# Performance work log

Measured on AMD Instinct MI355X. Metric: run time of the kernel, lower is better.

The kernel has to match this reference:

```python
import jax, jax.numpy as jnp
import numpy as np

NUM_EXPERTS = 8
TOP_K = 2
N_EMBD = 1024
BLOCKING = 128
D_FFN = ((4 * N_EMBD // TOP_K) + BLOCKING - 1) // BLOCKING * BLOCKING  # 2048


def setup_inputs() -> dict:
    key = jax.random.key(0)
    k_x, k_r, k_w1, k_w2 = jax.random.split(key, 4)
    B, S = 4, 2048
    x = jax.random.normal(k_x, (B, S, N_EMBD), dtype=jnp.float32)
    # nn.Linear weight layout: [out_features, in_features]
    router_w = jax.random.normal(k_r, (NUM_EXPERTS, N_EMBD), dtype=jnp.float32) * 0.02
    # trunc_normal(std=0.02, a=-0.06, b=0.06) approximated by clipped normal
    w1 = jnp.clip(jax.random.normal(k_w1, (N_EMBD, NUM_EXPERTS * D_FFN), dtype=jnp.float32) * 0.02, -0.06, 0.06)
    w2 = jnp.clip(jax.random.normal(k_w2, (NUM_EXPERTS * D_FFN, N_EMBD), dtype=jnp.float32) * 0.02, -0.06, 0.06)
    return {"x": x, "router_w": router_w, "w1": w1, "w2": w2}


def reference(x, router_w, w1, w2):
    B, S, D = x.shape
    T = B * S
    x_flat = x.reshape(T, D)

    # Router
    router_logits = x_flat @ router_w.T                       # [T, E]
    router_probs = jax.nn.softmax(router_logits.astype(jnp.float32), axis=-1)
    expert_weights, selected_experts = jax.lax.top_k(router_probs, TOP_K)  # [T, K]
    expert_weights = expert_weights / expert_weights.sum(axis=-1, keepdims=True)
    expert_weights = expert_weights.astype(x.dtype)

    # Combine weights c[t, e] = sum_k weight[t, k] * [sel[t, k] == e]
    combine = jnp.zeros((T, NUM_EXPERTS), dtype=x.dtype)
    combine = combine.at[jnp.arange(T)[:, None], selected_experts].add(expert_weights)

    # Expert FFNs (math equivalent of block-sparse sdd/gelu/dsd + scatter-combine)
    w1r = w1.reshape(D, NUM_EXPERTS, D_FFN)
    w2r = w2.reshape(NUM_EXPERTS, D_FFN, D)
    out_flat = jnp.zeros((T, D), dtype=x.dtype)
    for e in range(NUM_EXPERTS):
        h = jax.nn.gelu(x_flat @ w1r[:, e, :], approximate=False)  # [T, d_ffn]
        out_flat = out_flat + combine[:, e:e + 1] * (h @ w2r[e])
    output = out_flat.reshape(B, S, D)

    # Aux losses
    router_z_loss = jnp.mean(jax.nn.logsumexp(router_logits, axis=-1) ** 2)
    p_i = router_probs.mean(axis=0)                           # [E]
    f_i = jnp.zeros((NUM_EXPERTS,), dtype=x.dtype).at[selected_experts.reshape(-1)].add(
        jnp.float32(1.0) / (T * TOP_K))
    load_balance_loss = NUM_EXPERTS * jnp.dot(f_i, p_i.astype(x.dtype))

    return output, router_z_loss, load_balance_loss, f_i
```

## Files before the change

### kernel.cpp

```cpp
#include <hip/hip_runtime.h>
#include <hip/hip_bf16.h>
#include <math.h>

#define T_TOK   8192
#define D_MODEL 1024
#define DFFN    2048
#define N_EXP   8
#define NASSIGN (T_TOK*2)

#define BM 128
#define BN 128
#define BK 64
#define TILE_MAX 144

#define WS_ZSUM     0
#define WS_PSUM     4
#define WS_COUNTS   64
#define WS_CURSOR   96
#define WS_OFFS     128
#define WS_NTILES   160
#define WS_TMAP     256
#define WS_SEL      4096
#define WS_WGT      69632
#define WS_AIDX     135168
#define WS_AW       200704
#define WS_XB       266240
#define WS_W1T      (WS_XB + 16777216)
#define WS_W2T      (WS_W1T + 33554432)
#define WS_H        (WS_W2T + 33554432)

typedef __attribute__((ext_vector_type(8))) short bf16x8;
typedef __attribute__((ext_vector_type(4))) float f32x4;
typedef __attribute__((ext_vector_type(4))) unsigned int u32x4;

static __device__ __forceinline__ unsigned short f2bf(float f) {
    unsigned int u = __builtin_bit_cast(unsigned int, f);
    u += 0x7fffu + ((u >> 16) & 1u);
    return (unsigned short)(u >> 16);
}

static __device__ __forceinline__ void gll16(const unsigned short* g, unsigned short* l) {
    __builtin_amdgcn_global_load_lds(
        (const __attribute__((address_space(1))) unsigned int*)g,
        (__attribute__((address_space(3))) unsigned int*)l, 16, 0, 0);
}

static __device__ __forceinline__ int frag_off(int row, int kc) {
    return (row * 8 + (kc ^ (row & 7))) * 8;
}

__global__ __launch_bounds__(256) void transpose_cvt_kernel(
    const float* __restrict__ in, unsigned short* __restrict__ out, int K, int N)
{
    int e = blockIdx.z;
    const float* inp = in + (size_t)e * K * N;
    unsigned short* outp = out + (size_t)e * K * N;
    __shared__ unsigned short tile[64][68];
    int k0 = blockIdx.y * 64, n0 = blockIdx.x * 64;
    int tid = threadIdx.x;
    int r = tid >> 4, c4 = (tid & 15) * 4;
    #pragma unroll
    for (int p = 0; p < 4; ++p) {
        int k = r + p * 16;
        float4 v = *(const float4*)(inp + (size_t)(k0 + k) * N + n0 + c4);
        tile[k][c4+0] = f2bf(v.x);
        tile[k][c4+1] = f2bf(v.y);
        tile[k][c4+2] = f2bf(v.z);
        tile[k][c4+3] = f2bf(v.w);
    }
    __syncthreads();
    int n = tid >> 2, kc = (tid & 3) * 16;
    unsigned short t[16];
    #pragma unroll
    for (int j = 0; j < 16; ++j) t[j] = tile[kc + j][n];
    unsigned short* o = outp + (size_t)(n0 + n) * K + k0 + kc;
    *(u32x4*)o       = *(u32x4*)t;
    *(u32x4*)(o + 8) = *(u32x4*)(t + 8);
}

__global__ __launch_bounds__(256) void router_kernel(
    const float* __restrict__ x, const float* __restrict__ rw,
    float* zsum, float* psum, int* counts, int* sel, float* wgt,
    unsigned short* __restrict__ xb)
{
    __shared__ float xs[32*129];
    __shared__ float rs[8*129];
    __shared__ float lg[32*9];
    __shared__ float blk_p[8];
    __shared__ int   blk_c[8];
    __shared__ float blk_z;
    int tid = threadIdx.x;
    if (tid < 8) { blk_p[tid] = 0.f; blk_c[tid] = 0; }
    if (tid == 8) blk_z = 0.f;
    int tb = blockIdx.x * 32;
    int tt = tid >> 3, e = tid & 7;
    float acc = 0.f;
    for (int c = 0; c < 8; ++c) {
        int c0 = c * 128;
        #pragma unroll
        for (int p = 0; p < 16; ++p) {
            int flat = p * 256 + tid;
            int r = flat >> 7, col = flat & 127;
            xs[r*129 + col] = x[(size_t)(tb + r)*D_MODEL + c0 + col];
        }
        #pragma unroll
        for (int p = 0; p < 4; ++p) {
            int flat = p * 256 + tid;
            int er = flat >> 7, col = flat & 127;
            rs[er*129 + col] = rw[(size_t)er*D_MODEL + c0 + col];
        }
        __syncthreads();
        {
            int rr = tid >> 3, cc = (tid & 7) * 16;
            unsigned short tmp[16];
            #pragma unroll
            for (int j = 0; j < 16; ++j) tmp[j] = f2bf(xs[rr*129 + cc + j]);
            unsigned short* o = xb + (size_t)(tb + rr)*D_MODEL + c0 + cc;
            *(u32x4*)o       = *(u32x4*)tmp;
            *(u32x4*)(o + 8) = *(u32x4*)(tmp + 8);
        }
        #pragma unroll 8
        for (int i = 0; i < 128; ++i)
            acc += xs[tt*129 + i] * rs[e*129 + i];
        __syncthreads();
    }
    lg[tt*9 + e] = acc;
    __syncthreads();
    if (tid < 32) {
        int t = tb + tid;
        float l[8], p[8];
        float mx = -1e30f;
        #pragma unroll
        for (int j = 0; j < 8; ++j) { l[j] = lg[tid*9 + j]; mx = fmaxf(mx, l[j]); }
        float se = 0.f;
        #pragma unroll
        for (int j = 0; j < 8; ++j) { p[j] = expf(l[j] - mx); se += p[j]; }
        float inv = 1.f / se;
        #pragma unroll
        for (int j = 0; j < 8; ++j) p[j] *= inv;
        float lse = mx + logf(se);
        atomicAdd(&blk_z, lse*lse);
        #pragma unroll
        for (int j = 0; j < 8; ++j) atomicAdd(&blk_p[j], p[j]);
        int i0 = 0; float b0 = p[0];
        #pragma unroll
        for (int j = 1; j < 8; ++j) if (p[j] > b0) { b0 = p[j]; i0 = j; }
        int i1 = -1; float b1 = -1.f;
        #pragma unroll
        for (int j = 0; j < 8; ++j) if (j != i0 && p[j] > b1) { b1 = p[j]; i1 = j; }
        float s = b0 + b1;
        sel[t*2+0] = i0; sel[t*2+1] = i1;
        wgt[t*2+0] = b0 / s; wgt[t*2+1] = b1 / s;
        atomicAdd(&blk_c[i0], 1); atomicAdd(&blk_c[i1], 1);
    }
    __syncthreads();
    if (tid < 8) {
        atomicAdd(&counts[tid], blk_c[tid]);
        unsafeAtomicAdd(&psum[tid], blk_p[tid]);
    }
    if (tid == 8) unsafeAtomicAdd(zsum, blk_z);
}

__global__ void finalize_kernel(const int* counts, const float* psum, const float* zsum,
                                int* offs, int* ntiles, int* tmap, float* out_tail)
{
    if (threadIdx.x != 0) return;
    int off = 0, nt = 0;
    float lb = 0.f;
    for (int e = 0; e < N_EXP; ++e) {
        int c = counts[e];
        offs[e] = off;
        for (int m0 = 0; m0 < c; m0 += BM) {
            tmap[nt*4+0] = e;
            tmap[nt*4+1] = off + m0;
            tmap[nt*4+2] = min(BM, c - m0);
            tmap[nt*4+3] = 0;
            nt++;
        }
        float fi = (float)c / (float)NASSIGN;
        out_tail[2 + e] = fi;
        lb += fi * (psum[e] / (float)T_TOK);
        off += c;
    }
    *ntiles = nt;
    out_tail[0] = zsum[0] / (float)T_TOK;
    out_tail[1] = (float)N_EXP * lb;
}

__global__ __launch_bounds__(256) void scatter_kernel(
    const int* __restrict__ sel, const float* __restrict__ wgt,
    const int* __restrict__ offs, int* cursor, int* aidx, float* aw)
{
    int t = blockIdx.x * 256 + threadIdx.x;
    if (t >= T_TOK) return;
    #pragma unroll
    for (int k = 0; k < 2; ++k) {
        int e = sel[t*2 + k];
        int pos = atomicAdd(&cursor[e], 1);
        int r = offs[e] + pos;
        aidx[r] = t;
        aw[r] = wgt[t*2 + k];
    }
}

__global__ __launch_bounds__(256) void gemm1_kernel(
    const unsigned short* __restrict__ xb, const unsigned short* __restrict__ w1t,
    const int* __restrict__ aidx, const int* __restrict__ tmap,
    const int* __restrict__ ntiles, unsigned short* __restrict__ H)
{
    int tile = blockIdx.y;
    if (tile >= *ntiles) return;
    int e     = tmap[tile*4+0];
    int gr    = tmap[tile*4+1];
    int valid = tmap[tile*4+2];
    int n0 = blockIdx.x * BN;
    __shared__ unsigned short As[BM*BK];
    __shared__ unsigned short Bs[BN*BK];
    int tid = threadIdx.x;
    int lane = tid & 63, wave = tid >> 6;
    int wm = (wave & 1) * 64, wn = (wave >> 1) * 64;
    int q = lane >> 4, r16 = lane & 15;
    f32x4 acc[4][4];
    #pragma unroll
    for (int i = 0; i < 4; ++i)
        #pragma unroll
        for (int j = 0; j < 4; ++j) acc[i][j] = (f32x4){0.f, 0.f, 0.f, 0.f};

    const unsigned short* aga[4];
    const unsigned short* bga[4];
    unsigned short* ldsA[4];
    unsigned short* ldsB[4];
    #pragma unroll
    for (int j = 0; j < 4; ++j) {
        int c = tid + j*256;
        int m = c >> 3, kl = c & 7;
        int kg = kl ^ (m & 7);
        int tok = aidx[gr + min(m, valid - 1)];
        aga[j] = xb + (size_t)tok * D_MODEL + kg*8;
        bga[j] = w1t + ((size_t)(e * DFFN + n0 + m)) * D_MODEL + kg*8;
        ldsA[j] = As + c*8;
        ldsB[j] = Bs + c*8;
    }

    for (int kt = 0; kt < D_MODEL / BK; ++kt) {
        int ko = kt * BK;
        #pragma unroll
        for (int j = 0; j < 4; ++j) gll16(aga[j] + ko, ldsA[j]);
        #pragma unroll
        for (int j = 0; j < 4; ++j) gll16(bga[j] + ko, ldsB[j]);
        __syncthreads();
        #pragma unroll
        for (int kh = 0; kh < 2; ++kh) {
            bf16x8 af[4], bfr[4];
            #pragma unroll
            for (int im = 0; im < 4; ++im)
                af[im] = *(const bf16x8*)&As[frag_off(wm + im*16 + r16, q + 4*kh)];
            #pragma unroll
            for (int in = 0; in < 4; ++in)
                bfr[in] = *(const bf16x8*)&Bs[frag_off(wn + in*16 + r16, q + 4*kh)];
            #pragma unroll
            for (int im = 0; im < 4; ++im)
                #pragma unroll
                for (int in = 0; in < 4; ++in)
                    acc[im][in] = __builtin_amdgcn_mfma_f32_16x16x32_bf16(af[im], bfr[in], acc[im][in], 0, 0, 0);
        }
        __syncthreads();
    }
    #pragma unroll
    for (int im = 0; im < 4; ++im) {
        #pragma unroll
        for (int reg = 0; reg < 4; ++reg) {
            int m = wm + im*16 + q*4 + reg;
            if (m < valid) {
                size_t rowbase = (size_t)(gr + m) * DFFN + n0 + wn;
                #pragma unroll
                for (int in = 0; in < 4; ++in) {
                    float v = acc[im][in][reg];
                    float g = 0.5f * v * (1.0f + erff(v * 0.70710678118654752f));
                    H[rowbase + in*16 + r16] = f2bf(g);
                }
            }
        }
    }
}

__global__ __launch_bounds__(256) void gemm2_kernel(
    const unsigned short* __restrict__ H, const unsigned short* __restrict__ w2t,
    const int* __restrict__ aidx, const float* __restrict__ aw,
    const int* __restrict__ tmap, const int* __restrict__ ntiles,
    float* __restrict__ out)
{
    int tile = blockIdx.y;
    if (tile >= *ntiles) return;
    int e     = tmap[tile*4+0];
    int gr    = tmap[tile*4+1];
    int valid = tmap[tile*4+2];
    int n0 = blockIdx.x * BN;
    __shared__ unsigned short As[BM*BK];
    __shared__ unsigned short Bs[BN*BK];
    int tid = threadIdx.x;
    int lane = tid & 63, wave = tid >> 6;
    int wm = (wave & 1) * 64, wn = (wave >> 1) * 64;
    int q = lane >> 4, r16 = lane & 15;
    f32x4 acc[4][4];
    #pragma unroll
    for (int i = 0; i < 4; ++i)
        #pragma unroll
        for (int j = 0; j < 4; ++j) acc[i][j] = (f32x4){0.f, 0.f, 0.f, 0.f};

    const unsigned short* aga[4];
    const unsigned short* bga[4];
    unsigned short* ldsA[4];
    unsigned short* ldsB[4];
    #pragma unroll
    for (int j = 0; j < 4; ++j) {
        int c = tid + j*256;
        int m = c >> 3, kl = c & 7;
        int kg = kl ^ (m & 7);
        aga[j] = H + (size_t)(gr + min(m, valid - 1)) * DFFN + kg*8;
        bga[j] = w2t + (size_t)e * (DFFN * D_MODEL) + (size_t)(n0 + m) * DFFN + kg*8;
        ldsA[j] = As + c*8;
        ldsB[j] = Bs + c*8;
    }

    for (int kt = 0; kt < DFFN / BK; ++kt) {
        int ko = kt * BK;
        #pragma unroll
        for (int j = 0; j < 4; ++j) gll16(aga[j] + ko, ldsA[j]);
        #pragma unroll
        for (int j = 0; j < 4; ++j) gll16(bga[j] + ko, ldsB[j]);
        __syncthreads();
        #pragma unroll
        for (int kh = 0; kh < 2; ++kh) {
            bf16x8 af[4], bfr[4];
            #pragma unroll
            for (int im = 0; im < 4; ++im)
                af[im] = *(const bf16x8*)&As[frag_off(wm + im*16 + r16, q + 4*kh)];
            #pragma unroll
            for (int in = 0; in < 4; ++in)
                bfr[in] = *(const bf16x8*)&Bs[frag_off(wn + in*16 + r16, q + 4*kh)];
            #pragma unroll
            for (int im = 0; im < 4; ++im)
                #pragma unroll
                for (int in = 0; in < 4; ++in)
                    acc[im][in] = __builtin_amdgcn_mfma_f32_16x16x32_bf16(af[im], bfr[in], acc[im][in], 0, 0, 0);
        }
        __syncthreads();
    }
    #pragma unroll
    for (int im = 0; im < 4; ++im) {
        #pragma unroll
        for (int reg = 0; reg < 4; ++reg) {
            int m = wm + im*16 + q*4 + reg;
            if (m < valid) {
                int t = aidx[gr + m];
                float w = aw[gr + m];
                float* orow = out + (size_t)t*D_MODEL + n0 + wn;
                #pragma unroll
                for (int in = 0; in < 4; ++in)
                    unsafeAtomicAdd(&orow[in*16 + r16], w * acc[im][in][reg]);
            }
        }
    }
}

extern "C" void kernel_launch(void* const* d_in, const int* in_sizes, int n_in,
                              void* d_out, int out_size, void* d_ws, size_t ws_size,
                              hipStream_t stream)
{
    const float* x  = (const float*)d_in[0];
    const float* rw = (const float*)d_in[1];
    const float* w1 = (const float*)d_in[2];
    const float* w2 = (const float*)d_in[3];
    float* out = (float*)d_out;
    char* ws = (char*)d_ws;
    float* zsum   = (float*)(ws + WS_ZSUM);
    float* psum   = (float*)(ws + WS_PSUM);
    int*   counts = (int*)(ws + WS_COUNTS);
    int*   cursor = (int*)(ws + WS_CURSOR);
    int*   offs   = (int*)(ws + WS_OFFS);
    int*   ntiles = (int*)(ws + WS_NTILES);
    int*   tmap   = (int*)(ws + WS_TMAP);
    int*   sel    = (int*)(ws + WS_SEL);
    float* wgt    = (float*)(ws + WS_WGT);
    int*   aidx   = (int*)(ws + WS_AIDX);
    float* aw     = (float*)(ws + WS_AW);
    unsigned short* xb  = (unsigned short*)(ws + WS_XB);
    unsigned short* w1t = (unsigned short*)(ws + WS_W1T);
    unsigned short* w2t = (unsigned short*)(ws + WS_W2T);
    unsigned short* H   = (unsigned short*)(ws + WS_H);

    hipMemsetAsync(d_out, 0, (size_t)T_TOK * D_MODEL * sizeof(float), stream);
    hipMemsetAsync(ws, 0, 256, stream);

    transpose_cvt_kernel<<<dim3(16384/64, 1024/64, 1), 256, 0, stream>>>(w1, w1t, 1024, 16384);
    transpose_cvt_kernel<<<dim3(1024/64, 2048/64, 8), 256, 0, stream>>>(w2, w2t, 2048, 1024);

    router_kernel<<<T_TOK/32, 256, 0, stream>>>(x, rw, zsum, psum, counts, sel, wgt, xb);
    finalize_kernel<<<1, 64, 0, stream>>>(counts, psum, zsum, offs, ntiles, tmap,
                                          out + (size_t)T_TOK * D_MODEL);
    scatter_kernel<<<T_TOK/256, 256, 0, stream>>>(sel, wgt, offs, cursor, aidx, aw);
    gemm1_kernel<<<dim3(DFFN/BN, TILE_MAX), 256, 0, stream>>>(xb, w1t, aidx, tmap, ntiles, H);
    gemm2_kernel<<<dim3(D_MODEL/BN, TILE_MAX), 256, 0, stream>>>(H, w2t, aidx, aw, tmap, ntiles, out);
}
```

Measured before the change: 595.7 us.

## Double-buffer LDS in expert GEMMs and remap blocks for XCD locality

Both expert GEMM kernels now use double-buffered shared memory tiles: the next K-slice is prefetched with direct global-to-LDS loads while MFMAs run on the current slice, with explicit vmcnt waits and raw barriers in place of two __syncthreads per iteration. The grid is flattened to 1D and block IDs are remapped so that all N-tiles of a given row tile land on the same XCD, improving L2 reuse of the gathered activation rows. Wave priority is raised around the MFMA section. Doubling LDS per block lowers the number of resident blocks per CU, and the hand-written waitcnt counts assume eight outstanding loads per thread.

```diff
diff --git a/kernel.cpp b/kernel.cpp
--- a/kernel.cpp
+++ b/kernel.cpp
@@ -208,14 +208,17 @@
     const int* __restrict__ aidx, const int* __restrict__ tmap,
     const int* __restrict__ ntiles, unsigned short* __restrict__ H)
 {
-    int tile = blockIdx.y;
+    int bid = blockIdx.x;
+    int xcd = bid & 7;
+    int jj  = bid >> 3;
+    int tile = (jj >> 4) * 8 + xcd;
+    int n0   = (jj & 15) * BN;
     if (tile >= *ntiles) return;
     int e     = tmap[tile*4+0];
     int gr    = tmap[tile*4+1];
     int valid = tmap[tile*4+2];
-    int n0 = blockIdx.x * BN;
-    __shared__ unsigned short As[BM*BK];
-    __shared__ unsigned short Bs[BN*BK];
+    __shared__ unsigned short As[2][BM*BK];
+    __shared__ unsigned short Bs[2][BN*BK];
     int tid = threadIdx.x;
     int lane = tid & 63, wave = tid >> 6;
     int wm = (wave & 1) * 64, wn = (wave >> 1) * 64;
@@ -228,43 +231,62 @@
 
     const unsigned short* aga[4];
     const unsigned short* bga[4];
-    unsigned short* ldsA[4];
-    unsigned short* ldsB[4];
-    #pragma unroll
-    for (int j = 0; j < 4; ++j) {
-        int c = tid + j*256;
-        int m = c >> 3, kl = c & 7;
+    int coff[4];
+    #pragma unroll
+    for (int u = 0; u < 4; ++u) {
+        int cc = tid + u*256;
+        int m = cc >> 3, kl = cc & 7;
         int kg = kl ^ (m & 7);
         int tok = aidx[gr + min(m, valid - 1)];
-        aga[j] = xb + (size_t)tok * D_MODEL + kg*8;
-        bga[j] = w1t + ((size_t)(e * DFFN + n0 + m)) * D_MODEL + kg*8;
-        ldsA[j] = As + c*8;
-        ldsB[j] = Bs + c*8;
-    }
-
-    for (int kt = 0; kt < D_MODEL / BK; ++kt) {
-        int ko = kt * BK;
-        #pragma unroll
-        for (int j = 0; j < 4; ++j) gll16(aga[j] + ko, ldsA[j]);
-        #pragma unroll
-        for (int j = 0; j < 4; ++j) gll16(bga[j] + ko, ldsB[j]);
-        __syncthreads();
+        aga[u] = xb + (size_t)tok * D_MODEL + kg*8;
+        bga[u] = w1t + ((size_t)(e * DFFN + n0 + m)) * D_MODEL + kg*8;
+        coff[u] = cc * 8;
+    }
+
+    const int NK = D_MODEL / BK;
+    #pragma unroll
+    for (int u = 0; u < 4; ++u) gll16(aga[u], &As[0][coff[u]]);
+    #pragma unroll
+    for (int u = 0; u < 4; ++u) gll16(bga[u], &Bs[0][coff[u]]);
+
+    int cur = 0;
+    for (int kt = 0; kt < NK; ++kt) {
+        if (kt + 1 < NK) {
+            int ko = (kt + 1) * BK;
+            #pragma unroll
+            for (int u = 0; u < 4; ++u) gll16(aga[u] + ko, &As[cur^1][coff[u]]);
+            #pragma unroll
+            for (int u = 0; u < 4; ++u) gll16(bga[u] + ko, &Bs[cur^1][coff[u]]);
+            asm volatile("s_waitcnt vmcnt(8)" ::: "memory");
+        } else {
+            asm volatile("s_waitcnt vmcnt(0)" ::: "memory");
+        }
+        __builtin_amdgcn_sched_barrier(0);
+        __builtin_amdgcn_s_barrier();
+        asm volatile("" ::: "memory");
+        const unsigned short* Ab = &As[cur][0];
+        const unsigned short* Bb = &Bs[cur][0];
+        __builtin_amdgcn_s_setprio(1);
         #pragma unroll
         for (int kh = 0; kh < 2; ++kh) {
             bf16x8 af[4], bfr[4];
             #pragma unroll
             for (int im = 0; im < 4; ++im)
-                af[im] = *(const bf16x8*)&As[frag_off(wm + im*16 + r16, q + 4*kh)];
+                af[im] = *(const bf16x8*)&Ab[frag_off(wm + im*16 + r16, q + 4*kh)];
             #pragma unroll
             for (int in = 0; in < 4; ++in)
-                bfr[in] = *(const bf16x8*)&Bs[frag_off(wn + in*16 + r16, q + 4*kh)];
+                bfr[in] = *(const bf16x8*)&Bb[frag_off(wn + in*16 + r16, q + 4*kh)];
             #pragma unroll
             for (int im = 0; im < 4; ++im)
                 #pragma unroll
                 for (int in = 0; in < 4; ++in)
                     acc[im][in] = __builtin_amdgcn_mfma_f32_16x16x32_bf16(af[im], bfr[in], acc[im][in], 0, 0, 0);
         }
-        __syncthreads();
+        __builtin_amdgcn_s_setprio(0);
+        asm volatile("" ::: "memory");
+        __builtin_amdgcn_sched_barrier(0);
+        __builtin_amdgcn_s_barrier();
+        cur ^= 1;
     }
     #pragma unroll
     for (int im = 0; im < 4; ++im) {
@@ -290,14 +312,17 @@
     const int* __restrict__ tmap, const int* __restrict__ ntiles,
     float* __restrict__ out)
 {
-    int tile = blockIdx.y;
+    int bid = blockIdx.x;
+    int xcd = bid & 7;
+    int jj  = bid >> 3;
+    int tile = (jj >> 3) * 8 + xcd;
+    int n0   = (jj & 7) * BN;
     if (tile >= *ntiles) return;
     int e     = tmap[tile*4+0];
     int gr    = tmap[tile*4+1];
     int valid = tmap[tile*4+2];
-    int n0 = blockIdx.x * BN;
-    __shared__ unsigned short As[BM*BK];
-    __shared__ unsigned short Bs[BN*BK];
+    __shared__ unsigned short As[2][BM*BK];
+    __shared__ unsigned short Bs[2][BN*BK];
     int tid = threadIdx.x;
     int lane = tid & 63, wave = tid >> 6;
     int wm = (wave & 1) * 64, wn = (wave >> 1) * 64;
@@ -310,42 +335,61 @@
 
     const unsigned short* aga[4];
     const unsigned short* bga[4];
-    unsigned short* ldsA[4];
-    unsigned short* ldsB[4];
-    #pragma unroll
-    for (int j = 0; j < 4; ++j) {
-        int c = tid + j*256;
-        int m = c >> 3, kl = c & 7;
+    int coff[4];
+    #pragma unroll
+    for (int u = 0; u < 4; ++u) {
+        int cc = tid + u*256;
+        int m = cc >> 3, kl = cc & 7;
         int kg = kl ^ (m & 7);
-        aga[j] = H + (size_t)(gr + min(m, valid - 1)) * DFFN + kg*8;
-        bga[j] = w2t + (size_t)e * (DFFN * D_MODEL) + (size_t)(n0 + m) * DFFN + kg*8;
-        ldsA[j] = As + c*8;
-        ldsB[j] = Bs + c*8;
-    }
-
-    for (int kt = 0; kt < DFFN / BK; ++kt) {
-        int ko = kt * BK;
-        #pragma unroll
-        for (int j = 0; j < 4; ++j) gll16(aga[j] + ko, ldsA[j]);
-        #pragma unroll
-        for (int j = 0; j < 4; ++j) gll16(bga[j] + ko, ldsB[j]);
-        __syncthreads();
+        aga[u] = H + (size_t)(gr + min(m, valid - 1)) * DFFN + kg*8;
+        bga[u] = w2t + (size_t)e * (DFFN * D_MODEL) + (size_t)(n0 + m) * DFFN + kg*8;
+        coff[u] = cc * 8;
+    }
+
+    const int NK = DFFN / BK;
+    #pragma unroll
+    for (int u = 0; u < 4; ++u) gll16(aga[u], &As[0][coff[u]]);
+    #pragma unroll
+    for (int u = 0; u < 4; ++u) gll16(bga[u], &Bs[0][coff[u]]);
+
+    int cur = 0;
+    for (int kt = 0; kt < NK; ++kt) {
+        if (kt + 1 < NK) {
+            int ko = (kt + 1) * BK;
+            #pragma unroll
+            for (int u = 0; u < 4; ++u) gll16(aga[u] + ko, &As[cur^1][coff[u]]);
+            #pragma unroll
+            for (int u = 0; u < 4; ++u) gll16(bga[u] + ko, &Bs[cur^1][coff[u]]);
+            asm volatile("s_waitcnt vmcnt(8)" ::: "memory");
+        } else {
+            asm volatile("s_waitcnt vmcnt(0)" ::: "memory");
+        }
+        __builtin_amdgcn_sched_barrier(0);
+        __builtin_amdgcn_s_barrier();
+        asm volatile("" ::: "memory");
+        const unsigned short* Ab = &As[cur][0];
+        const unsigned short* Bb = &Bs[cur][0];
+        __builtin_amdgcn_s_setprio(1);
         #pragma unroll
         for (int kh = 0; kh < 2; ++kh) {
             bf16x8 af[4], bfr[4];
             #pragma unroll
             for (int im = 0; im < 4; ++im)
-                af[im] = *(const bf16x8*)&As[frag_off(wm + im*16 + r16, q + 4*kh)];
+                af[im] = *(const bf16x8*)&Ab[frag_off(wm + im*16 + r16, q + 4*kh)];
             #pragma unroll
             for (int in = 0; in < 4; ++in)
-                bfr[in] = *(const bf16x8*)&Bs[frag_off(wn + in*16 + r16, q + 4*kh)];
+                bfr[in] = *(const bf16x8*)&Bb[frag_off(wn + in*16 + r16, q + 4*kh)];
             #pragma unroll
             for (int im = 0; im < 4; ++im)
                 #pragma unroll
                 for (int in = 0; in < 4; ++in)
                     acc[im][in] = __builtin_amdgcn_mfma_f32_16x16x32_bf16(af[im], bfr[in], acc[im][in], 0, 0, 0);
         }
-        __syncthreads();
+        __builtin_amdgcn_s_setprio(0);
+        asm volatile("" ::: "memory");
+        __builtin_amdgcn_sched_barrier(0);
+        __builtin_amdgcn_s_barrier();
+        cur ^= 1;
     }
     #pragma unroll
     for (int im = 0; im < 4; ++im) {
@@ -400,6 +444,6 @@
     finalize_kernel<<<1, 64, 0, stream>>>(counts, psum, zsum, offs, ntiles, tmap,
                                           out + (size_t)T_TOK * D_MODEL);
     scatter_kernel<<<T_TOK/256, 256, 0, stream>>>(sel, wgt, offs, cursor, aidx, aw);
-    gemm1_kernel<<<dim3(DFFN/BN, TILE_MAX), 256, 0, stream>>>(xb, w1t, aidx, tmap, ntiles, H);
-    gemm2_kernel<<<dim3(D_MODEL/BN, TILE_MAX), 256, 0, stream>>>(H, w2t, aidx, aw, tmap, ntiles, out);
-}
+    gemm1_kernel<<<dim3(TILE_MAX * (DFFN/BN)), 256, 0, stream>>>(xb, w1t, aidx, tmap, ntiles, H);
+    gemm2_kernel<<<dim3(TILE_MAX * (D_MODEL/BN)), 256, 0, stream>>>(H, w2t, aidx, aw, tmap, ntiles, out);
+}
```

After: 580.1 us. -2.6%, faster.
